# Performance work log

Hardware: AMD Instinct MI355X
Metric: run time of the kernel (lower is better)

The kernel has to match this reference:

```python
import jax, jax.numpy as jnp
import numpy as np

N, K, D = 524288, 32, 8
EPS = 1e-6


def setup_inputs() -> dict:
    key = jax.random.key(0)
    k1, k2, k3, k4 = jax.random.split(key, 4)
    x = jax.random.normal(k1, (N, D), dtype=jnp.float32)
    pi = jax.random.uniform(k2, (K,), dtype=jnp.float32)
    means = jax.random.normal(k3, (K, D), dtype=jnp.float32)
    # eye + small perturbation keeps tril(chol_var) well-conditioned (PD covariance)
    chol_var = jnp.eye(D, dtype=jnp.float32)[None] + 0.1 * jax.random.normal(k4, (K, D, D), dtype=jnp.float32)
    return {"x": x, "pi": pi, "means": means, "chol_var": chol_var}


def reference(x, pi, means, chol_var):
    d = x.shape[-1]
    L = jnp.tril(chol_var)                                   # [K,d,d]
    cov = jnp.einsum('kij,klj->kil', L, L) + EPS * jnp.eye(d, dtype=x.dtype)
    C = jnp.linalg.cholesky(cov)                             # [K,d,d] (MVN recomputes cholesky)
    logdet = 2.0 * jnp.sum(jnp.log(jnp.diagonal(C, axis1=-2, axis2=-1)), axis=-1)  # [K]
    eye = jnp.eye(d, dtype=x.dtype)
    Cinv = jax.vmap(lambda c: jax.scipy.linalg.solve_triangular(c, eye, lower=True))(C)  # [K,d,d]
    zx = jnp.einsum('kij,nj->nki', Cinv, x)                  # [N,K,d]
    zm = jnp.einsum('kij,kj->ki', Cinv, means)               # [K,d]
    maha = jnp.sum((zx - zm[None]) ** 2, axis=-1)            # [N,K]
    log_2pi = jnp.log(2.0 * jnp.pi).astype(x.dtype)
    log_probs = -0.5 * (maha + d * log_2pi + logdet[None])   # [N,K]
    wll = log_probs + jax.nn.log_softmax(pi)[None]
    return jax.scipy.special.logsumexp(wll, axis=1)          # [N]
```

## Files before the change

### kernel.cpp

```cpp
#include <hip/hip_runtime.h>
#include <math.h>

#define K_ 32
#define D_ 8
#define CSTRIDE 48
#define S_ 4

typedef __attribute__((ext_vector_type(16))) float f32x16;

__global__ void gmm_precompute(const float* __restrict__ pi,
                               const float* __restrict__ means,
                               const float* __restrict__ chol,
                               float* __restrict__ cv) {
    int k = threadIdx.x;
    if (k >= K_) return;

    float L[D_][D_];
#pragma unroll
    for (int i = 0; i < D_; ++i)
#pragma unroll
        for (int j = 0; j <= i; ++j)
            L[i][j] = chol[k * D_ * D_ + i * D_ + j];

    float rd[D_];
#pragma unroll
    for (int i = 0; i < D_; ++i) rd[i] = 1.f / L[i][i];

    float Ci[D_][D_];
#pragma unroll
    for (int j = 0; j < D_; ++j) {
        Ci[j][j] = rd[j];
#pragma unroll
        for (int i = j + 1; i < D_; ++i) {
            float s = 0.f;
#pragma unroll
            for (int m = j; m < i; ++m) s += L[i][m] * Ci[m][j];
            Ci[i][j] = -s * rd[i];
        }
    }

    float logdet = 0.f;
#pragma unroll
    for (int i = 0; i < D_; ++i) logdet += __logf(fabsf(L[i][i]));
    logdet *= 2.f;

    float zm[D_];
#pragma unroll
    for (int i = 0; i < D_; ++i) {
        float s = 0.f;
#pragma unroll
        for (int j = 0; j <= i; ++j) s += Ci[i][j] * means[k * D_ + j];
        zm[i] = s;
    }

    float mx = pi[0];
#pragma unroll
    for (int t = 1; t < K_; ++t) mx = fmaxf(mx, pi[t]);
    float se = 0.f;
#pragma unroll
    for (int t = 0; t < K_; ++t) se += __expf(pi[t] - mx);
    float lse = mx + __logf(se);

    const float LOG2PI = 1.8378770664093453f;
    const float SQH = 0.70710678118654752f;
    float cst = (pi[k] - lse) - 0.5f * (logdet + (float)D_ * LOG2PI);

    float* p = cv + k * CSTRIDE;
    int t = 0;
#pragma unroll
    for (int i = 0; i < D_; ++i)
#pragma unroll
        for (int j = 0; j <= i; ++j) p[t++] = Ci[i][j] * SQH;
#pragma unroll
    for (int i = 0; i < D_; ++i) p[36 + i] = zm[i] * SQH;
    p[44] = cst;
    p[45] = 0.f; p[46] = 0.f; p[47] = 0.f;
}

#define CC(j) ((j) < 16 ? c0[(j)] : ((j) < 32 ? c1[(j) - 16] : c2[(j) - 32]))

__global__ __launch_bounds__(256) void gmm_main(const float* __restrict__ x,
                                                const float* __restrict__ cv,
                                                float* __restrict__ out, int N) {
    const int q = N >> 2;
    const int t = blockIdx.x * 256 + threadIdx.x;
    if (t >= q) return;

    float xv[S_][D_];
#pragma unroll
    for (int s = 0; s < S_; ++s) {
        const float4* xp = (const float4*)x + (size_t)(t + s * q) * 2;
        float4 a = xp[0], b = xp[1];
        xv[s][0] = a.x; xv[s][1] = a.y; xv[s][2] = a.z; xv[s][3] = a.w;
        xv[s][4] = b.x; xv[s][5] = b.y; xv[s][6] = b.z; xv[s][7] = b.w;
    }

    float m[S_], sm[S_];
#pragma unroll
    for (int s = 0; s < S_; ++s) { m[s] = -INFINITY; sm[s] = 0.f; }

#pragma unroll 1
    for (int k = 0; k < K_; ++k) {
        const unsigned long long p =
            (unsigned long long)(const void*)(cv + k * CSTRIDE);
        f32x16 c0, c1, c2;
        asm("s_load_dwordx16 %0, %3, 0x0\n\t"
            "s_load_dwordx16 %1, %3, 0x40\n\t"
            "s_load_dwordx16 %2, %3, 0x80\n\t"
            "s_waitcnt lgkmcnt(0)"
            : "=&s"(c0), "=&s"(c1), "=&s"(c2)
            : "s"(p));

        float w[S_];
#pragma unroll
        for (int s = 0; s < S_; ++s) w[s] = CC(44);
        int tt = 0;
#pragma unroll
        for (int i = 0; i < D_; ++i) {
            float z[S_];
#pragma unroll
            for (int s = 0; s < S_; ++s) z[s] = -CC(36 + i);
#pragma unroll
            for (int j = 0; j <= i; ++j)
#pragma unroll
                for (int s = 0; s < S_; ++s)
                    z[s] = fmaf(CC(tt + j), xv[s][j], z[s]);
            tt += i + 1;
#pragma unroll
            for (int s = 0; s < S_; ++s) w[s] = fmaf(-z[s], z[s], w[s]);
        }

#pragma unroll
        for (int s = 0; s < S_; ++s) {
            float d = w[s] - m[s];
            float e = __expf(-fabsf(d));
            sm[s] = (d > 0.f) ? fmaf(sm[s], e, 1.f) : (sm[s] + e);
            m[s] = fmaxf(m[s], w[s]);
        }
    }

#pragma unroll
    for (int s = 0; s < S_; ++s)
        out[t + s * q] = m[s] + __logf(sm[s]);
}

extern "C" void kernel_launch(void* const* d_in, const int* in_sizes, int n_in,
                              void* d_out, int out_size, void* d_ws, size_t ws_size,
                              hipStream_t stream) {
    const float* x     = (const float*)d_in[0];
    const float* pi    = (const float*)d_in[1];
    const float* means = (const float*)d_in[2];
    const float* chol  = (const float*)d_in[3];
    float* out = (float*)d_out;
    float* cv  = (float*)d_ws;

    int N = in_sizes[0] / D_;

    gmm_precompute<<<1, 64, 0, stream>>>(pi, means, chol, cv);
    int q = N >> 2;
    gmm_main<<<(q + 255) / 256, 256, 0, stream>>>(x, cv, out, N);
}
```

Measured before the change: 87.31 us.

## Fuse precompute into main kernel with per-block LDS constants and base-2 exp

Removes the separate precompute launch: every block now has 32 threads recompute the per-component inverse Cholesky, logdet and constants into shared memory, then syncs before the main loop. The main loop reads the constants from LDS as float4 vector loads instead of scalar s_load, and the scale factors are folded so the log-sum-exp runs in base 2 (exp2f/log2f) with a final multiply by ln2. This removes one launch and its dependency gap at the cost of redundant per-block triangular inversion and a barrier, and turns the uniform constant reads into LDS reads that go through VGPRs instead of SGPRs.

```diff
diff --git a/kernel.cpp b/kernel.cpp
--- a/kernel.cpp
+++ b/kernel.cpp
@@ -6,84 +6,85 @@
 #define CSTRIDE 48
 #define S_ 4
 
-typedef __attribute__((ext_vector_type(16))) float f32x16;
+__global__ __launch_bounds__(256) void gmm_fused(
+    const float* __restrict__ x,
+    const float* __restrict__ pi,
+    const float* __restrict__ means,
+    const float* __restrict__ chol,
+    float* __restrict__ out, int N)
+{
+    __shared__ float cv[K_ * CSTRIDE];
 
-__global__ void gmm_precompute(const float* __restrict__ pi,
-                               const float* __restrict__ means,
-                               const float* __restrict__ chol,
-                               float* __restrict__ cv) {
-    int k = threadIdx.x;
-    if (k >= K_) return;
+    const int tid = threadIdx.x;
+    if (tid < K_) {
+        const int k = tid;
 
-    float L[D_][D_];
+        float L[D_][D_];
 #pragma unroll
-    for (int i = 0; i < D_; ++i)
+        for (int i = 0; i < D_; ++i)
 #pragma unroll
-        for (int j = 0; j <= i; ++j)
-            L[i][j] = chol[k * D_ * D_ + i * D_ + j];
+            for (int j = 0; j <= i; ++j)
+                L[i][j] = chol[k * D_ * D_ + i * D_ + j];
 
-    float rd[D_];
+        float rd[D_];
 #pragma unroll
-    for (int i = 0; i < D_; ++i) rd[i] = 1.f / L[i][i];
+        for (int i = 0; i < D_; ++i) rd[i] = 1.f / L[i][i];
 
-    float Ci[D_][D_];
+        float Ci[D_][D_];
 #pragma unroll
-    for (int j = 0; j < D_; ++j) {
-        Ci[j][j] = rd[j];
+        for (int j = 0; j < D_; ++j) {
+            Ci[j][j] = rd[j];
 #pragma unroll
-        for (int i = j + 1; i < D_; ++i) {
+            for (int i = j + 1; i < D_; ++i) {
+                float s = 0.f;
+#pragma unroll
+                for (int m = j; m < i; ++m) s += L[i][m] * Ci[m][j];
+                Ci[i][j] = -s * rd[i];
+            }
+        }
+
+        float logdet = 0.f;
+#pragma unroll
+        for (int i = 0; i < D_; ++i) logdet += __logf(fabsf(L[i][i]));
+        logdet *= 2.f;
+
+        float zm[D_];
+#pragma unroll
+        for (int i = 0; i < D_; ++i) {
             float s = 0.f;
 #pragma unroll
-            for (int m = j; m < i; ++m) s += L[i][m] * Ci[m][j];
-            Ci[i][j] = -s * rd[i];
+            for (int j = 0; j <= i; ++j) s += Ci[i][j] * means[k * D_ + j];
+            zm[i] = s;
         }
+
+        float mx = pi[0];
+#pragma unroll
+        for (int t = 1; t < K_; ++t) mx = fmaxf(mx, pi[t]);
+        float se = 0.f;
+#pragma unroll
+        for (int t = 0; t < K_; ++t) se += __expf(pi[t] - mx);
+        float lse = mx + __logf(se);
+
+        const float LOG2PI = 1.8378770664093453f;
+        const float LOG2E  = 1.4426950408889634f;
+        const float SQH2   = 0.84932180028801905f;
+        float cst2 = ((pi[k] - lse) - 0.5f * (logdet + (float)D_ * LOG2PI)) * LOG2E;
+
+        float* p = cv + k * CSTRIDE;
+        int t = 0;
+#pragma unroll
+        for (int i = 0; i < D_; ++i)
+#pragma unroll
+            for (int j = 0; j <= i; ++j) p[t++] = Ci[i][j] * SQH2;
+#pragma unroll
+        for (int i = 0; i < D_; ++i) p[36 + i] = zm[i] * SQH2;
+        p[44] = cst2;
+        p[45] = 0.f; p[46] = 0.f; p[47] = 0.f;
     }
+    __syncthreads();
 
-    float logdet = 0.f;
-#pragma unroll
-    for (int i = 0; i < D_; ++i) logdet += __logf(fabsf(L[i][i]));
-    logdet *= 2.f;
-
-    float zm[D_];
-#pragma unroll
-    for (int i = 0; i < D_; ++i) {
-        float s = 0.f;
-#pragma unroll
-        for (int j = 0; j <= i; ++j) s += Ci[i][j] * means[k * D_ + j];
-        zm[i] = s;
-    }
-
-    float mx = pi[0];
-#pragma unroll
-    for (int t = 1; t < K_; ++t) mx = fmaxf(mx, pi[t]);
-    float se = 0.f;
-#pragma unroll
-    for (int t = 0; t < K_; ++t) se += __expf(pi[t] - mx);
-    float lse = mx + __logf(se);
-
-    const float LOG2PI = 1.8378770664093453f;
-    const float SQH = 0.70710678118654752f;
-    float cst = (pi[k] - lse) - 0.5f * (logdet + (float)D_ * LOG2PI);
-
-    float* p = cv + k * CSTRIDE;
-    int t = 0;
-#pragma unroll
-    for (int i = 0; i < D_; ++i)
-#pragma unroll
-        for (int j = 0; j <= i; ++j) p[t++] = Ci[i][j] * SQH;
-#pragma unroll
-    for (int i = 0; i < D_; ++i) p[36 + i] = zm[i] * SQH;
-    p[44] = cst;
-    p[45] = 0.f; p[46] = 0.f; p[47] = 0.f;
-}
-
-#define CC(j) ((j) < 16 ? c0[(j)] : ((j) < 32 ? c1[(j) - 16] : c2[(j) - 32]))
-
-__global__ __launch_bounds__(256) void gmm_main(const float* __restrict__ x,
-                                                const float* __restrict__ cv,
-                                                float* __restrict__ out, int N) {
     const int q = N >> 2;
-    const int t = blockIdx.x * 256 + threadIdx.x;
+    const int t = blockIdx.x * 256 + tid;
     if (t >= q) return;
 
     float xv[S_][D_];
@@ -101,30 +102,28 @@
 
 #pragma unroll 1
     for (int k = 0; k < K_; ++k) {
-        const unsigned long long p =
-            (unsigned long long)(const void*)(cv + k * CSTRIDE);
-        f32x16 c0, c1, c2;
-        asm("s_load_dwordx16 %0, %3, 0x0\n\t"
-            "s_load_dwordx16 %1, %3, 0x40\n\t"
-            "s_load_dwordx16 %2, %3, 0x80\n\t"
-            "s_waitcnt lgkmcnt(0)"
-            : "=&s"(c0), "=&s"(c1), "=&s"(c2)
-            : "s"(p));
+        float c[CSTRIDE];
+        {
+            const float4* ps = (const float4*)(cv + k * CSTRIDE);
+            float4* cd = (float4*)c;
+#pragma unroll
+            for (int qq = 0; qq < 12; ++qq) cd[qq] = ps[qq];
+        }
 
         float w[S_];
 #pragma unroll
-        for (int s = 0; s < S_; ++s) w[s] = CC(44);
+        for (int s = 0; s < S_; ++s) w[s] = c[44];
         int tt = 0;
 #pragma unroll
         for (int i = 0; i < D_; ++i) {
             float z[S_];
 #pragma unroll
-            for (int s = 0; s < S_; ++s) z[s] = -CC(36 + i);
+            for (int s = 0; s < S_; ++s) z[s] = -c[36 + i];
 #pragma unroll
             for (int j = 0; j <= i; ++j)
 #pragma unroll
                 for (int s = 0; s < S_; ++s)
-                    z[s] = fmaf(CC(tt + j), xv[s][j], z[s]);
+                    z[s] = fmaf(c[tt + j], xv[s][j], z[s]);
             tt += i + 1;
 #pragma unroll
             for (int s = 0; s < S_; ++s) w[s] = fmaf(-z[s], z[s], w[s]);
@@ -133,15 +132,16 @@
 #pragma unroll
         for (int s = 0; s < S_; ++s) {
             float d = w[s] - m[s];
-            float e = __expf(-fabsf(d));
+            float e = exp2f(-fabsf(d));
             sm[s] = (d > 0.f) ? fmaf(sm[s], e, 1.f) : (sm[s] + e);
             m[s] = fmaxf(m[s], w[s]);
         }
     }
 
+    const float LN2 = 0.69314718055994531f;
 #pragma unroll
     for (int s = 0; s < S_; ++s)
-        out[t + s * q] = m[s] + __logf(sm[s]);
+        out[t + s * q] = (m[s] + log2f(sm[s])) * LN2;
 }
 
 extern "C" void kernel_launch(void* const* d_in, const int* in_sizes, int n_in,
@@ -152,11 +152,9 @@
     const float* means = (const float*)d_in[2];
     const float* chol  = (const float*)d_in[3];
     float* out = (float*)d_out;
-    float* cv  = (float*)d_ws;
 
     int N = in_sizes[0] / D_;
+    int q = N >> 2;
 
-    gmm_precompute<<<1, 64, 0, stream>>>(pi, means, chol, cv);
-    int q = N >> 2;
-    gmm_main<<<(q + 255) / 256, 256, 0, stream>>>(x, cv, out, N);
+    gmm_fused<<<(q + 255) / 256, 256, 0, stream>>>(x, pi, means, chol, out, N);
 }
```

Result: no change. 88.87 us (+1.8%).
